# Optimization experiments

Measured on AMD Instinct MI355X. Metric: run time of the kernel, lower is better.

## Reference

```python
import jax, jax.numpy as jnp
import numpy as np

B, LQ, LK, D = 4, 2048, 2048, 1024
H = 16  # num_heads == num_kv_heads (only runnable config of the source module)
HD = D // H  # 64


def setup_inputs() -> dict:
    key = jax.random.key(0)
    ks = jax.random.split(key, 4)
    std = 0.02
    return {
        "x": jax.random.normal(ks[0], (B, LQ, D), dtype=jnp.float32),
        "text_input": jax.random.normal(ks[1], (B, LK, D), dtype=jnp.float32),
        "Wq": jax.random.normal(ks[2], (D, D), dtype=jnp.float32) * std,
        "bq": jnp.zeros((D,), dtype=jnp.float32),
        "Wkv": jax.random.normal(ks[3], (D, 2 * D), dtype=jnp.float32) * std,
        "bkv": jnp.zeros((2 * D,), dtype=jnp.float32),
    }


def reference(x, text_input, Wq, bq, Wkv, bkv):
    b, lq, d = x.shape
    lk = text_input.shape[1]
    # projections
    Q = x @ Wq + bq                       # [b, lq, d]
    KV = text_input @ Wkv + bkv           # [b, lk, 2d]
    K, V = jnp.split(KV, 2, axis=-1)      # [b, lk, d] each
    # split heads (num_kv_heads == num_heads, so repeat_interleave is identity)
    Q = Q.reshape(b, lq, H, HD)
    K = K.reshape(b, lk, H, HD)
    V = V.reshape(b, lk, H, HD)
    # scaled dot-product attention
    scale = 1.0 / jnp.sqrt(jnp.asarray(HD, dtype=Q.dtype))
    scores = jnp.einsum("bqhd,bkhd->bhqk", Q, K) * scale  # [b, H, lq, lk]
    attn = jax.nn.softmax(scores, axis=-1)
    out = jnp.einsum("bhqk,bkhd->bqhd", attn, V)          # [b, lq, H, HD]
    # dropout p=0.0 (eval) -> identity
    return out.reshape(b, lq, d)
```

## Files before the change

### kernel.cpp

```cpp
#include <hip/hip_runtime.h>
#include <hip/hip_bf16.h>


typedef unsigned short u16;
typedef unsigned int u32;

typedef __attribute__((ext_vector_type(8))) __bf16 bf16x8;
typedef __attribute__((ext_vector_type(2))) _Float16 f16x2;
typedef __attribute__((ext_vector_type(8))) _Float16 f16x8;
typedef __attribute__((ext_vector_type(4))) float f32x4;
typedef __attribute__((ext_vector_type(16))) float f32x16;
typedef __attribute__((ext_vector_type(4))) float f4;
typedef __attribute__((ext_vector_type(4))) unsigned short u16x4;
typedef __attribute__((ext_vector_type(4))) unsigned int u32x4;

#define DEVI __device__ __forceinline__

DEVI u16 f2b(float f) {
  u32 u = __float_as_uint(f);
  return (u16)((u + 0x7fffu + ((u >> 16) & 1u)) >> 16);
}

DEVI u16 f2h(float f) {
  _Float16 h = (_Float16)f;
  return __builtin_bit_cast(u16, h);
}

DEVI f16x2 pk_f16(float a, float b) {
  return __builtin_bit_cast(f16x2, __builtin_amdgcn_cvt_pkrtz(a, b));
}

DEVI u32 cvt_pk_bf16(float a, float b) {
  u32 r;
  asm("v_cvt_pk_bf16_f32 %0, %1, %2" : "=v"(r) : "v"(a), "v"(b));
  return r;
}

DEVI void gld_lds16(void* lds, const void* g) {
  __builtin_amdgcn_global_load_lds(
      (const __attribute__((address_space(1))) u32*)g,
      (__attribute__((address_space(3))) u32*)lds, 16, 0, 0);
}

__global__ __launch_bounds__(256) void k_prep(
    const float* __restrict__ Wq, const float* __restrict__ Wkv,
    u16* __restrict__ WQT, u16* __restrict__ WKVT) {
  __shared__ float tile[32][33];
  const int bid = blockIdx.x, tid = threadIdx.x;
  const float* in;
  u16* out;
  int N, bx, by;
  if (bid < 1024) {
    in = Wq; out = WQT; N = 1024; bx = bid & 31; by = bid >> 5;
  } else {
    int b2 = bid - 1024; in = Wkv; out = WKVT; N = 2048; bx = b2 & 63; by = b2 >> 6;
  }
  const int K = 1024;
  const int n0 = bx * 32, k0 = by * 32;
  const int tx = tid & 31, ty = tid >> 5;
#pragma unroll
  for (int j = 0; j < 32; j += 8)
    tile[ty + j][tx] = in[(size_t)(k0 + ty + j) * N + n0 + tx];
  __syncthreads();
#pragma unroll
  for (int j = 0; j < 32; j += 8)
    out[(size_t)(n0 + ty + j) * K + k0 + tx] = f2b(tile[tx][ty + j]);
}

__global__ __launch_bounds__(256) void k_gemm(
    const float* __restrict__ X, const float* __restrict__ TXT,
    const u16* __restrict__ WQT, const u16* __restrict__ WKVT,
    const float* __restrict__ bq, const float* __restrict__ bkv,
    u16* __restrict__ QG, u16* __restrict__ KG, u16* __restrict__ VG) {
  __shared__ alignas(16) char As[2][8192];
  __shared__ alignas(16) char Bs[2][8192];
  const int bid0 = blockIdx.x;
  const int bid = (bid0 & 7) * 192 + (bid0 >> 3);
  const int tid = threadIdx.x;
  const int w = tid >> 6, l = tid & 63;
  const int wr = w >> 1, wc = w & 1;

  const bool isQ = bid < 512;
  int nb, mb;
  const float* Af32;
  const u16* Bptr;
  const float* bias;
  if (isQ) {
    nb = bid & 7; mb = bid >> 3; Af32 = X; Bptr = WQT; bias = bq;
  } else {
    int b2 = bid - 512; nb = b2 & 15; mb = b2 >> 4; Af32 = TXT; Bptr = WKVT; bias = bkv;
  }
  const int m0 = mb << 7, n0 = nb << 7;

  u32 doff[2], bsoff[2], fsoff[2];
#pragma unroll
  for (int i = 0; i < 2; i++) {
    u32 o = (u32)(i * 4096 + tid * 16);
    u32 row = o >> 6;
    u32 csw = (o & 63) ^ (((row >> 1) & 3) << 4);
    doff[i] = o;
    bsoff[i] = row * 2048 + csw;
    fsoff[i] = row * 4096 + 2 * csw;
  }
  const char* Abase = (const char*)Af32 + (size_t)m0 * 4096;
  const char* Borig = (const char*)Bptr + (size_t)n0 * 2048;

  f32x16 acc[2][2];
#pragma unroll
  for (int i = 0; i < 2; i++)
#pragma unroll
    for (int j = 0; j < 2; j++)
#pragma unroll
      for (int e = 0; e < 16; e++) acc[i][j][e] = 0.f;

  const u32 xk = (u32)((l >> 1) & 3);
  const u32 hi5 = (u32)(l >> 5);
  const u32 arow0 = (u32)(wr * 64 + (l & 31)) * 64;
  const u32 brow0 = (u32)(wc * 64 + (l & 31)) * 64;

#pragma unroll
  for (int i = 0; i < 2; i++) {
    gld_lds16(&Bs[0][doff[i]], Borig + bsoff[i]);
    f4 a0 = *(const f4*)(Abase + fsoff[i]);
    f4 a1 = *(const f4*)(Abase + fsoff[i] + 16);
    u32x4 pk;
    pk.x = cvt_pk_bf16(a0.x, a0.y);
    pk.y = cvt_pk_bf16(a0.z, a0.w);
    pk.z = cvt_pk_bf16(a1.x, a1.y);
    pk.w = cvt_pk_bf16(a1.z, a1.w);
    *(u32x4*)&As[0][doff[i]] = pk;
  }
  __syncthreads();

  int buf = 0;
  for (int kt = 0; kt < 32; kt++) {
    f4 a0[2], a1[2];
    if (kt < 31) {
#pragma unroll
      for (int i = 0; i < 2; i++) {
        gld_lds16(&Bs[buf ^ 1][doff[i]], Borig + (u32)(kt + 1) * 64 + bsoff[i]);
        a0[i] = *(const f4*)(Abase + (u32)(kt + 1) * 128 + fsoff[i]);
        a1[i] = *(const f4*)(Abase + (u32)(kt + 1) * 128 + fsoff[i] + 16);
      }
    }
    bf16x8 af[2][2], bfr[2][2];
#pragma unroll
    for (int i = 0; i < 2; i++)
#pragma unroll
      for (int h = 0; h < 2; h++) {
        const u32 co = (((u32)(2 * h) + hi5) ^ xk) << 4;
        af[i][h] = *(const bf16x8*)&As[buf][arow0 + (u32)i * 2048 + co];
        bfr[i][h] = *(const bf16x8*)&Bs[buf][brow0 + (u32)i * 2048 + co];
      }
#pragma unroll
    for (int i = 0; i < 2; i++)
#pragma unroll
      for (int j = 0; j < 2; j++)
#pragma unroll
        for (int h = 0; h < 2; h++)
          acc[i][j] = __builtin_amdgcn_mfma_f32_32x32x16_bf16(af[i][h], bfr[j][h], acc[i][j], 0, 0, 0);
    if (kt < 31) {
#pragma unroll
      for (int i = 0; i < 2; i++) {
        u32x4 pk;
        pk.x = cvt_pk_bf16(a0[i].x, a0[i].y);
        pk.y = cvt_pk_bf16(a0[i].z, a0[i].w);
        pk.z = cvt_pk_bf16(a1[i].x, a1[i].y);
        pk.w = cvt_pk_bf16(a1[i].z, a1[i].w);
        *(u32x4*)&As[buf ^ 1][doff[i]] = pk;
      }
    }
    __syncthreads();
    buf ^= 1;
  }

#pragma unroll
  for (int i = 0; i < 2; i++)
#pragma unroll
    for (int j = 0; j < 2; j++) {
      const int n = n0 + wc * 64 + j * 32 + (l & 31);
      const float bv = bias[n];
#pragma unroll
      for (int rg = 0; rg < 4; rg++) {
        const int mbase = m0 + wr * 64 + i * 32 + rg * 8 + ((l >> 5) << 2);
        const int bb = mbase >> 11;
        const int mrow = mbase & 2047;
        float a0 = acc[i][j][rg * 4 + 0] + bv;
        float a1 = acc[i][j][rg * 4 + 1] + bv;
        float a2 = acc[i][j][rg * 4 + 2] + bv;
        float a3 = acc[i][j][rg * 4 + 3] + bv;
        if (isQ) {
          const int h = n >> 6, hd = n & 63;
          u16* dst = QG + ((((size_t)bb * 16 + h) * 2048 + mrow) << 6) + hd;
          dst[0] = f2b(a0 * 0.18033688011112042f);
          dst[64] = f2b(a1 * 0.18033688011112042f);
          dst[128] = f2b(a2 * 0.18033688011112042f);
          dst[192] = f2b(a3 * 0.18033688011112042f);
        } else if (n < 1024) {
          const int h = n >> 6, d = n & 63;
          char* base = (char*)KG + ((((size_t)bb * 16 + h) * 2048 + mrow) << 7);
          float av[4] = {a0, a1, a2, a3};
#pragma unroll
          for (int r = 0; r < 4; r++) {
            u32 off = (u32)r * 128 + (((u32)d * 2) ^ (((u32)(mrow + r) & 7) << 4));
            *(u16*)(base + off) = f2b(av[r]);
          }
        } else {
          const int nn = n - 1024;
          const int h = nn >> 6, hd = nn & 63;
          u16x4 pk;
          pk.x = f2h(a0); pk.y = f2h(a1); pk.z = f2h(a2); pk.w = f2h(a3);
          char* base = (char*)VG + (((size_t)bb * 16 + h) << 18);
          u32 off = ((u32)(mrow >> 6) << 13) + (((u32)(mrow >> 5) & 1) << 12) +
                    ((u32)(hd >> 4) << 10) + (((u32)(mrow >> 2) & 3) << 8) +
                    ((u32)(hd & 15) << 4) + (((u32)(mrow >> 4) & 1) << 3);
          *(u16x4*)(base + off) = pk;
        }
      }
    }
}

__global__ __launch_bounds__(256) void k_attn(
    const u16* __restrict__ QG, const u16* __restrict__ KG, const u16* __restrict__ VG,
    float* __restrict__ out) {
  __shared__ alignas(16) char Ks[2][8192];
  __shared__ alignas(16) char Vs[2][8192];
  const int tid = threadIdx.x, w = tid >> 6, l = tid & 63;
  const int g = l >> 4, q = l & 15;
  const int bid = blockIdx.x;
  const int orig = (bid & 7) * 128 + (bid >> 3);
  const int qt = orig & 15;
  const int hh = (orig >> 4) & 15;
  const int b = orig >> 8;
  const size_t bh = (size_t)b * 16 + hh;

  const int qrowA = qt * 128 + w * 16 + q;
  const int qrowB = qrowA + 64;

  const u16* QpA = QG + ((bh * 2048 + (size_t)qrowA) << 6) + (g << 3);
  const u16* QpB = QG + ((bh * 2048 + (size_t)qrowB) << 6) + (g << 3);
  const bf16x8 qf0a = *(const bf16x8*)QpA;
  const bf16x8 qf1a = *(const bf16x8*)(QpA + 32);
  const bf16x8 qf0b = *(const bf16x8*)QpB;
  const bf16x8 qf1b = *(const bf16x8*)(QpB + 32);

  const char* Kbase = (const char*)KG + (bh << 18);
  const char* Vbase = (const char*)VG + (bh << 18);

  f32x4 lsA = (f32x4){0.f, 0.f, 0.f, 0.f};
  f32x4 lsB = (f32x4){0.f, 0.f, 0.f, 0.f};
  f32x4 oa[4], ob4[4];
#pragma unroll
  for (int c = 0; c < 4; c++) {
    oa[c] = (f32x4){0.f, 0.f, 0.f, 0.f};
    ob4[c] = (f32x4){0.f, 0.f, 0.f, 0.f};
  }
  f16x8 ones8;
#pragma unroll
  for (int e = 0; e < 8; e++) ones8[e] = (_Float16)1.0f;

  gld_lds16(&Ks[0][tid * 16], Kbase + tid * 16);
  gld_lds16(&Ks[0][4096 + tid * 16], Kbase + 4096 + tid * 16);
  gld_lds16(&Vs[0][tid * 16], Vbase + tid * 16);
  gld_lds16(&Vs[0][4096 + tid * 16], Vbase + 4096 + tid * 16);
  __syncthreads();

  const u32 ksw = ((u32)(l & 7)) << 4;
  const u32 kro = ((u32)q) << 7;
  const u32 kin = ((u32)g) << 4;

  auto body = [&](int BUF, int kb) {
    if (kb < 31) {
      const char* kp = Kbase + (size_t)(kb + 1) * 8192 + tid * 16;
      const char* vp = Vbase + (size_t)(kb + 1) * 8192 + tid * 16;
      gld_lds16(&Ks[BUF ^ 1][tid * 16], kp);
      gld_lds16(&Ks[BUF ^ 1][4096 + tid * 16], kp + 4096);
      gld_lds16(&Vs[BUF ^ 1][tid * 16], vp);
      gld_lds16(&Vs[BUF ^ 1][4096 + tid * 16], vp + 4096);
    }
    f32x4 sa[4], sb[4];
    __builtin_amdgcn_s_setprio(1);
#pragma unroll
    for (int t = 0; t < 4; t++) {
      const char* kr = &Ks[BUF][kro + (u32)t * 2048];
      bf16x8 kf0 = *(const bf16x8*)(kr + (kin ^ ksw));
      bf16x8 kf1 = *(const bf16x8*)(kr + ((kin + 64) ^ ksw));
      f32x4 z = (f32x4){0.f, 0.f, 0.f, 0.f};
      sa[t] = __builtin_amdgcn_mfma_f32_16x16x32_bf16(kf0, qf0a, z, 0, 0, 0);
      sa[t] = __builtin_amdgcn_mfma_f32_16x16x32_bf16(kf1, qf1a, sa[t], 0, 0, 0);
      sb[t] = __builtin_amdgcn_mfma_f32_16x16x32_bf16(kf0, qf0b, z, 0, 0, 0);
      sb[t] = __builtin_amdgcn_mfma_f32_16x16x32_bf16(kf1, qf1b, sb[t], 0, 0, 0);
    }
    __builtin_amdgcn_s_setprio(0);

    float pA[4][4], pB[4][4];
#pragma unroll
    for (int t = 0; t < 4; t++)
#pragma unroll
      for (int r = 0; r < 4; r++) {
        pA[t][r] = __builtin_amdgcn_exp2f(sa[t][r]);
        pB[t][r] = __builtin_amdgcn_exp2f(sb[t][r]);
      }

    __builtin_amdgcn_s_setprio(1);
#pragma unroll
    for (int u = 0; u < 2; u++) {
      f16x2 a0 = pk_f16(pA[2 * u][0], pA[2 * u][1]);
      f16x2 a1 = pk_f16(pA[2 * u][2], pA[2 * u][3]);
      f16x2 a2 = pk_f16(pA[2 * u + 1][0], pA[2 * u + 1][1]);
      f16x2 a3 = pk_f16(pA[2 * u + 1][2], pA[2 * u + 1][3]);
      f16x8 pfa;
      pfa[0] = a0.x; pfa[1] = a0.y; pfa[2] = a1.x; pfa[3] = a1.y;
      pfa[4] = a2.x; pfa[5] = a2.y; pfa[6] = a3.x; pfa[7] = a3.y;
      f16x2 b0 = pk_f16(pB[2 * u][0], pB[2 * u][1]);
      f16x2 b1 = pk_f16(pB[2 * u][2], pB[2 * u][3]);
      f16x2 b2 = pk_f16(pB[2 * u + 1][0], pB[2 * u + 1][1]);
      f16x2 b3 = pk_f16(pB[2 * u + 1][2], pB[2 * u + 1][3]);
      f16x8 pfb;
      pfb[0] = b0.x; pfb[1] = b0.y; pfb[2] = b1.x; pfb[3] = b1.y;
      pfb[4] = b2.x; pfb[5] = b2.y; pfb[6] = b3.x; pfb[7] = b3.y;
      lsA = __builtin_amdgcn_mfma_f32_16x16x32_f16(ones8, pfa, lsA, 0, 0, 0);
      lsB = __builtin_amdgcn_mfma_f32_16x16x32_f16(ones8, pfb, lsB, 0, 0, 0);
#pragma unroll
      for (int c = 0; c < 4; c++) {
        f16x8 vf = *(const f16x8*)&Vs[BUF][(u32)u * 4096 + (u32)c * 1024 + (u32)l * 16];
        oa[c] = __builtin_amdgcn_mfma_f32_16x16x32_f16(vf, pfa, oa[c], 0, 0, 0);
        ob4[c] = __builtin_amdgcn_mfma_f32_16x16x32_f16(vf, pfb, ob4[c], 0, 0, 0);
      }
    }
    __builtin_amdgcn_s_setprio(0);
    __syncthreads();
  };

  for (int kb2 = 0; kb2 < 16; kb2++) {
    body(0, 2 * kb2);
    body(1, 2 * kb2 + 1);
  }

  const float invA = 1.0f / lsA.x;
  const float invB = 1.0f / lsB.x;
  float* obA = out + ((size_t)b * 2048 + (size_t)qrowA) * 1024 + hh * 64;
  float* obB = out + ((size_t)b * 2048 + (size_t)qrowB) * 1024 + hh * 64;
#pragma unroll
  for (int c = 0; c < 4; c++) {
    f32x4 va = oa[c] * invA;
    f32x4 vb2 = ob4[c] * invB;
    *(f32x4*)(obA + c * 16 + g * 4) = va;
    *(f32x4*)(obB + c * 16 + g * 4) = vb2;
  }
}

extern "C" void kernel_launch(void* const* d_in, const int* in_sizes, int n_in,
                              void* d_out, int out_size, void* d_ws, size_t ws_size,
                              hipStream_t stream) {
  const float* x = (const float*)d_in[0];
  const float* text = (const float*)d_in[1];
  const float* Wq = (const float*)d_in[2];
  const float* bq = (const float*)d_in[3];
  const float* Wkv = (const float*)d_in[4];
  const float* bkv = (const float*)d_in[5];
  float* out = (float*)d_out;
  char* ws = (char*)d_ws;

  const size_t MiB = 1u << 20;
  u16* WQT = (u16*)(ws + 0 * MiB);
  u16* WKVT = (u16*)(ws + 2 * MiB);
  u16* QG = (u16*)(ws + 6 * MiB);
  u16* KG = (u16*)(ws + 22 * MiB);
  u16* VG = (u16*)(ws + 38 * MiB);

  k_prep<<<3072, 256, 0, stream>>>(Wq, Wkv, WQT, WKVT);
  k_gemm<<<1536, 256, 0, stream>>>(x, text, WQT, WKVT, bq, bkv, QG, KG, VG);
  k_attn<<<1024, 256, 0, stream>>>(QG, KG, VG, out);
}
```

Baseline: 168.1 us.

## Deepen projection GEMM pipeline to prefetch two K-tiles ahead

```diff
diff --git a/kernel.cpp b/kernel.cpp
--- a/kernel.cpp
+++ b/kernel.cpp
@@ -73,7 +73,7 @@
     const float* __restrict__ bq, const float* __restrict__ bkv,
     u16* __restrict__ QG, u16* __restrict__ KG, u16* __restrict__ VG) {
   __shared__ alignas(16) char As[2][8192];
-  __shared__ alignas(16) char Bs[2][8192];
+  __shared__ alignas(16) char Bs[4][8192];
   const int bid0 = blockIdx.x;
   const int bid = (bid0 & 7) * 192 + (bid0 >> 3);
   const int tid = threadIdx.x;
@@ -118,61 +118,80 @@
   const u32 arow0 = (u32)(wr * 64 + (l & 31)) * 64;
   const u32 brow0 = (u32)(wc * 64 + (l & 31)) * 64;
 
+  f4 sa0[2][2], sa1[2][2];
+
+#pragma unroll
+  for (int i = 0; i < 2; i++) gld_lds16(&Bs[0][doff[i]], Borig + bsoff[i]);
 #pragma unroll
   for (int i = 0; i < 2; i++) {
-    gld_lds16(&Bs[0][doff[i]], Borig + bsoff[i]);
-    f4 a0 = *(const f4*)(Abase + fsoff[i]);
-    f4 a1 = *(const f4*)(Abase + fsoff[i] + 16);
+    sa0[0][i] = *(const f4*)(Abase + fsoff[i]);
+    sa1[0][i] = *(const f4*)(Abase + fsoff[i] + 16);
+  }
+#pragma unroll
+  for (int i = 0; i < 2; i++) gld_lds16(&Bs[1][doff[i]], Borig + 64 + bsoff[i]);
+#pragma unroll
+  for (int i = 0; i < 2; i++) {
+    sa0[1][i] = *(const f4*)(Abase + 128 + fsoff[i]);
+    sa1[1][i] = *(const f4*)(Abase + 128 + fsoff[i] + 16);
+  }
+#pragma unroll
+  for (int i = 0; i < 2; i++) {
     u32x4 pk;
-    pk.x = cvt_pk_bf16(a0.x, a0.y);
-    pk.y = cvt_pk_bf16(a0.z, a0.w);
-    pk.z = cvt_pk_bf16(a1.x, a1.y);
-    pk.w = cvt_pk_bf16(a1.z, a1.w);
+    pk.x = cvt_pk_bf16(sa0[0][i].x, sa0[0][i].y);
+    pk.y = cvt_pk_bf16(sa0[0][i].z, sa0[0][i].w);
+    pk.z = cvt_pk_bf16(sa1[0][i].x, sa1[0][i].y);
+    pk.w = cvt_pk_bf16(sa1[0][i].z, sa1[0][i].w);
     *(u32x4*)&As[0][doff[i]] = pk;
   }
-  __syncthreads();
-
-  int buf = 0;
-  for (int kt = 0; kt < 32; kt++) {
-    f4 a0[2], a1[2];
-    if (kt < 31) {
-#pragma unroll
-      for (int i = 0; i < 2; i++) {
-        gld_lds16(&Bs[buf ^ 1][doff[i]], Borig + (u32)(kt + 1) * 64 + bsoff[i]);
-        a0[i] = *(const f4*)(Abase + (u32)(kt + 1) * 128 + fsoff[i]);
-        a1[i] = *(const f4*)(Abase + (u32)(kt + 1) * 128 + fsoff[i] + 16);
-      }
-    }
-    bf16x8 af[2][2], bfr[2][2];
-#pragma unroll
-    for (int i = 0; i < 2; i++)
-#pragma unroll
-      for (int h = 0; h < 2; h++) {
-        const u32 co = (((u32)(2 * h) + hi5) ^ xk) << 4;
-        af[i][h] = *(const bf16x8*)&As[buf][arow0 + (u32)i * 2048 + co];
-        bfr[i][h] = *(const bf16x8*)&Bs[buf][brow0 + (u32)i * 2048 + co];
-      }
-#pragma unroll
-    for (int i = 0; i < 2; i++)
-#pragma unroll
-      for (int j = 0; j < 2; j++)
-#pragma unroll
-        for (int h = 0; h < 2; h++)
-          acc[i][j] = __builtin_amdgcn_mfma_f32_32x32x16_bf16(af[i][h], bfr[j][h], acc[i][j], 0, 0, 0);
-    if (kt < 31) {
-#pragma unroll
-      for (int i = 0; i < 2; i++) {
-        u32x4 pk;
-        pk.x = cvt_pk_bf16(a0[i].x, a0[i].y);
-        pk.y = cvt_pk_bf16(a0[i].z, a0[i].w);
-        pk.z = cvt_pk_bf16(a1[i].x, a1[i].y);
-        pk.w = cvt_pk_bf16(a1[i].z, a1[i].w);
-        *(u32x4*)&As[buf ^ 1][doff[i]] = pk;
-      }
-    }
-    __syncthreads();
-    buf ^= 1;
-  }
+  asm volatile("s_waitcnt lgkmcnt(0)" ::: "memory");
+  __builtin_amdgcn_s_barrier();
+
+#define GEMM_BODY(KT, J, P)                                                        \
+  do {                                                                             \
+    const int kt = (KT);                                                           \
+    if (kt < 30) {                                                                 \
+      _Pragma("unroll") for (int i = 0; i < 2; i++)                                \
+          gld_lds16(&Bs[((J) + 2) & 3][doff[i]],                                   \
+                    Borig + (u32)(kt + 2) * 64 + bsoff[i]);                        \
+      _Pragma("unroll") for (int i = 0; i < 2; i++) {                              \
+        sa0[(P)][i] = *(const f4*)(Abase + (u32)(kt + 2) * 128 + fsoff[i]);        \
+        sa1[(P)][i] = *(const f4*)(Abase + (u32)(kt + 2) * 128 + fsoff[i] + 16);   \
+      }                                                                            \
+    }                                                                              \
+    if (kt < 31) {                      \
+      _Pragma("unroll") for (int i = 0; i < 2; i++) {                              \
+        u32x4 pk;                                                                  \
+        pk.x = cvt_pk_bf16(sa0[(P) ^ 1][i].x, sa0[(P) ^ 1][i].y);                  \
+        pk.y = cvt_pk_bf16(sa0[(P) ^ 1][i].z, sa0[(P) ^ 1][i].w);                  \
+        pk.z = cvt_pk_bf16(sa1[(P) ^ 1][i].x, sa1[(P) ^ 1][i].y);                  \
+        pk.w = cvt_pk_bf16(sa1[(P) ^ 1][i].z, sa1[(P) ^ 1][i].w);                  \
+        *(u32x4*)&As[(P) ^ 1][doff[i]] = pk;                                       \
+      }                                                                            \
+    }                                                                              \
+    bf16x8 af[2][2], bfr[2][2];                                                    \
+    _Pragma("unroll") for (int i = 0; i < 2; i++)                                  \
+        _Pragma("unroll") for (int h = 0; h < 2; h++) {                            \
+      const u32 co = (((u32)(2 * h) + hi5) ^ xk) << 4;                             \
+      af[i][h] = *(const bf16x8*)&As[(P)][arow0 + (u32)i * 2048 + co];             \
+      bfr[i][h] = *(const bf16x8*)&Bs[(J)][brow0 + (u32)i * 2048 + co];            \
+    }                                                                              \
+    _Pragma("unroll") for (int i = 0; i < 2; i++)                                  \
+        _Pragma("unroll") for (int j2 = 0; j2 < 2; j2++)                           \
+            _Pragma("unroll") for (int h = 0; h < 2; h++)                          \
+                acc[i][j2] = __builtin_amdgcn_mfma_f32_32x32x16_bf16(              \
+                    af[i][h], bfr[j2][h], acc[i][j2], 0, 0, 0);                    \
+    asm volatile("s_waitcnt lgkmcnt(0)" ::: "memory");                             \
+    __builtin_amdgcn_s_barrier();                                                  \
+  } while (0)
+
+  for (int k4 = 0; k4 < 8; k4++) {
+    const int kt0 = k4 * 4;
+    GEMM_BODY(kt0 + 0, 0, 0);
+    GEMM_BODY(kt0 + 1, 1, 1);
+    GEMM_BODY(kt0 + 2, 2, 0);
+    GEMM_BODY(kt0 + 3, 3, 1);
+  }
+#undef GEMM_BODY
 
 #pragma unroll
   for (int i = 0; i < 2; i++)
```

Measured after the change: 163.2 us. 2.9% less time.
